# Kernel optimization log

Measured on AMD Instinct MI355X. Metric: run time of the kernel, lower is better.

The kernel has to match this reference:

```python
import jax, jax.numpy as jnp
import numpy as np

N = 100000   # nodes
E = 2000000  # edges per etype
D = 256      # in_dim
C = 16       # num_classes (per-etype Linear out dim)
R = 4        # number of canonical etypes


def setup_inputs() -> dict:
    key = jax.random.key(0)
    k0, k1, k2, k3, k4, k5 = jax.random.split(key, 6)
    feat = jax.random.normal(k0, (N, D), dtype=jnp.float32)
    src_idx = jax.random.randint(k1, (R, E), 0, N, dtype=jnp.int32)
    dst_idx = jax.random.randint(k2, (R, E), 0, N, dtype=jnp.int32)
    eweight = jax.random.uniform(k3, (R, E, 1), dtype=jnp.float32)
    W = jax.random.normal(k4, (R, D, C), dtype=jnp.float32) / np.sqrt(D).astype(np.float32)
    b = jax.random.normal(k5, (R, C), dtype=jnp.float32) * 0.01
    return {"feat": feat, "src_idx": src_idx, "dst_idx": dst_idx,
            "eweight": eweight, "W": W, "b": b}


def reference(feat, src_idx, dst_idx, eweight, W, b):
    """Hetero GNN layer: per-etype Linear -> u_mul_e message -> mean reduce per
    dst node -> sum across etypes (DGL multi_update_all(..., 'sum'))."""
    n = feat.shape[0]

    def per_etype(Wr, br, src, dst, ew):
        wh = feat @ Wr + br                      # [N, C] per-etype linear
        m = jnp.take(wh, src, axis=0) * ew       # [E, C] u_mul_e message
        s = jax.ops.segment_sum(m, dst, num_segments=n)            # [N, C]
        cnt = jax.ops.segment_sum(jnp.ones((src.shape[0],), feat.dtype),
                                  dst, num_segments=n)             # [N]
        # DGL mean: nodes with no incoming messages contribute 0
        cnt = cnt[:, None]
        return jnp.where(cnt > 0, s / jnp.maximum(cnt, 1.0), jnp.zeros_like(s))

    h = jax.vmap(per_etype)(W, b, src_idx, dst_idx, eweight)  # [R, N, C]
    return h.sum(axis=0)                                       # cross-etype sum
```

## Files before the change

### kernel.cpp

```cpp
#include <hip/hip_runtime.h>

constexpr int N = 100000;
constexpr int E = 2000000;
constexpr int D = 256;
constexpr int C = 16;
constexpr int R = 4;
constexpr int NCOL = R * C;
constexpr int TOT = R * E;

constexpr int BKN = 256;
constexpr int NBUK = (N + BKN - 1) / BKN;
constexpr int EPB = 16384;
constexpr int NBLK = (E + EPB - 1) / EPB;
constexpr int NROWS = R * NBUK;
constexpr int HLEN = NROWS * NBLK;
constexpr int SCAN_ELEMS = 2048;
constexpr int SCAN_NBLK = (HLEN + SCAN_ELEMS - 1) / SCAN_ELEMS;
constexpr int CAP = 3328;
constexpr int CHK = 4096;
constexpr int AGRID = ((NBUK + 1) / 2) * 8;
constexpr int SGRID = ((NBLK + 1) / 2) * 8;

typedef __attribute__((ext_vector_type(8))) short short8;
typedef __attribute__((ext_vector_type(8))) unsigned short u16x8;
typedef __attribute__((ext_vector_type(4))) float f32x4;
typedef __attribute__((ext_vector_type(4))) int i32x4;

__device__ __forceinline__ float bf2f(unsigned short h) {
    return __uint_as_float(((unsigned int)h) << 16);
}
__device__ __forceinline__ unsigned short f2bf(float f) {
    unsigned int x = __float_as_uint(f);
    x += 0x7FFFu + ((x >> 16) & 1u);
    return (unsigned short)(x >> 16);
}

__global__ void wt_kernel(const float* __restrict__ W, short8* __restrict__ wtb) {
    const int idx = blockIdx.x * blockDim.x + threadIdx.x;
    if (idx >= 8 * 4 * 64) return;
    const int lane = idx & 63;
    const int ct   = (idx >> 6) & 3;
    const int ks   = idx >> 8;
    const int r = ct, c = lane & 15;
    const int kbase = ks * 32 + (lane >> 4) * 8;
    short8 v;
#pragma unroll
    for (int j = 0; j < 8; ++j)
        v[j] = (short)f2bf(W[(size_t)r * D * C + (size_t)(kbase + j) * C + c]);
    wtb[idx] = v;
}

__global__ __launch_bounds__(256) void gemm_kernel(
    const f32x4* __restrict__ feat4, const short8* __restrict__ wtb,
    const float* __restrict__ b, unsigned short* __restrict__ whb) {
    __shared__ unsigned short alds[64 * 272];
    const int t   = threadIdx.x;
    const int n0  = blockIdx.x * 64;

#pragma unroll
    for (int j = 0; j < 16; ++j) {
        const int idx = t + j * 256;
        const int row = idx >> 6, k4 = idx & 63;
        const int grow = n0 + row;
        const int lrow = (grow < N) ? grow : (N - 1);
        const f32x4 v = __builtin_nontemporal_load(&feat4[(size_t)lrow * 64 + k4]);
        ushort4 u;
        u.x = f2bf(v.x); u.y = f2bf(v.y); u.z = f2bf(v.z); u.w = f2bf(v.w);
        *(ushort4*)&alds[row * 272 + k4 * 4] = u;
    }
    __syncthreads();

    const int lane = t & 63;
    const int wv   = t >> 6;
    const int wrow = wv * 16 + (lane & 15);
    const int kblk = lane >> 4;

    f32x4 acc0 = {0.f, 0.f, 0.f, 0.f};
    f32x4 acc1 = acc0, acc2 = acc0, acc3 = acc0;

#pragma unroll
    for (int ks = 0; ks < 8; ++ks) {
        const short8 af = *(const short8*)&alds[wrow * 272 + ks * 32 + kblk * 8];
        const short8 b0 = wtb[(ks * 4 + 0) * 64 + lane];
        const short8 b1 = wtb[(ks * 4 + 1) * 64 + lane];
        const short8 b2 = wtb[(ks * 4 + 2) * 64 + lane];
        const short8 b3 = wtb[(ks * 4 + 3) * 64 + lane];
        acc0 = __builtin_amdgcn_mfma_f32_16x16x32_bf16(af, b0, acc0, 0, 0, 0);
        acc1 = __builtin_amdgcn_mfma_f32_16x16x32_bf16(af, b1, acc1, 0, 0, 0);
        acc2 = __builtin_amdgcn_mfma_f32_16x16x32_bf16(af, b2, acc2, 0, 0, 0);
        acc3 = __builtin_amdgcn_mfma_f32_16x16x32_bf16(af, b3, acc3, 0, 0, 0);
    }

    const int c    = lane & 15;
    const int rowb = n0 + wv * 16 + (lane >> 4) * 4;
    const float bias0 = b[ 0 + c];
    const float bias1 = b[16 + c];
    const float bias2 = b[32 + c];
    const float bias3 = b[48 + c];
#pragma unroll
    for (int reg = 0; reg < 4; ++reg) {
        const int gr = rowb + reg;
        if (gr < N) {
            whb[((size_t)0 * N + gr) * 16 + c] = f2bf(acc0[reg] + bias0);
            whb[((size_t)1 * N + gr) * 16 + c] = f2bf(acc1[reg] + bias1);
            whb[((size_t)2 * N + gr) * 16 + c] = f2bf(acc2[reg] + bias2);
            whb[((size_t)3 * N + gr) * 16 + c] = f2bf(acc3[reg] + bias3);
        }
    }
}

__global__ __launch_bounds__(256) void hist_kernel(const int* __restrict__ dst,
                                                   int* __restrict__ hist) {
    __shared__ int hcnt[NBUK];
    const int t = threadIdx.x;
    const int r = blockIdx.y;
    for (int i = t; i < NBUK; i += 256) hcnt[i] = 0;
    __syncthreads();
    const int e0 = blockIdx.x * EPB;
    if (E - e0 >= EPB) {
        const i32x4* d4 = (const i32x4*)(dst + (size_t)r * E + e0);
#pragma unroll
        for (int j = 0; j < EPB / 1024; ++j) {
            const i32x4 d = __builtin_nontemporal_load(&d4[t + j * 256]);
            atomicAdd(&hcnt[d.x >> 8], 1);
            atomicAdd(&hcnt[d.y >> 8], 1);
            atomicAdd(&hcnt[d.z >> 8], 1);
            atomicAdd(&hcnt[d.w >> 8], 1);
        }
    } else {
        const int* d = dst + (size_t)r * E;
        for (int e = e0 + t; e < E; e += 256)
            atomicAdd(&hcnt[d[e] >> 8], 1);
    }
    __syncthreads();
    for (int i = t; i < NBUK; i += 256)
        hist[(size_t)(r * NBUK + i) * NBLK + blockIdx.x] = hcnt[i];
}

__global__ __launch_bounds__(256) void scan1_kernel(int* __restrict__ data,
                                                    int* __restrict__ partials) {
    __shared__ int sh[256];
    const int t = threadIdx.x;
    const int idx = blockIdx.x * SCAN_ELEMS + t * 8;
    int v[8];
#pragma unroll
    for (int j = 0; j < 8; ++j)
        v[j] = (idx + j < HLEN) ? data[idx + j] : 0;
    int s = 0;
#pragma unroll
    for (int j = 0; j < 8; ++j) s += v[j];
    sh[t] = s;
    __syncthreads();
    for (int off = 1; off < 256; off <<= 1) {
        int x = (t >= off) ? sh[t - off] : 0;
        __syncthreads();
        sh[t] += x;
        __syncthreads();
    }
    int run = sh[t] - s;
    if (t == 255) partials[blockIdx.x] = sh[255];
#pragma unroll
    for (int j = 0; j < 8; ++j) {
        if (idx + j < HLEN) data[idx + j] = run;
        run += v[j];
    }
}

__global__ __launch_bounds__(1024) void scan2_kernel(int* __restrict__ partials, int n) {
    __shared__ int sh[1024];
    const int t = threadIdx.x;
    int a = (2 * t     < n) ? partials[2 * t]     : 0;
    int b = (2 * t + 1 < n) ? partials[2 * t + 1] : 0;
    const int s = a + b;
    sh[t] = s;
    __syncthreads();
    for (int off = 1; off < 1024; off <<= 1) {
        int x = (t >= off) ? sh[t - off] : 0;
        __syncthreads();
        sh[t] += x;
        __syncthreads();
    }
    const int excl = sh[t] - s;
    if (2 * t     < n) partials[2 * t]     = excl;
    if (2 * t + 1 < n) partials[2 * t + 1] = excl + a;
}

__global__ void scan3_kernel(int* __restrict__ data, const int* __restrict__ partials) {
    const int i = blockIdx.x * blockDim.x + threadIdx.x;
    if (i < HLEN) data[i] += partials[i / SCAN_ELEMS];
}

__global__ __launch_bounds__(512) void scatter_kernel(const int* __restrict__ src,
                                                      const int* __restrict__ dst,
                                                      const float* __restrict__ ew,
                                                      const int* __restrict__ hist,
                                                      int2* __restrict__ sorted) {
    __shared__ int2 lrec[CHK];
    __shared__ int  lidx[CHK];
    __shared__ short lbkt[CHK];
    __shared__ int gcur[NBUK];
    __shared__ int loff[NBUK + 1];
    __shared__ int lcnt[NBUK];
    const int t = threadIdx.x;
    const int s = blockIdx.x & 7;
    const int r = s >> 1;
    const int cb0 = (blockIdx.x >> 3) * 2 + (s & 1);
    if (cb0 >= NBLK) return;

    for (int i = t; i < NBUK; i += 512)
        gcur[i] = hist[(size_t)(r * NBUK + i) * NBLK + cb0];

    const int e0 = cb0 * EPB;
    const int e1 = min(e0 + EPB, E);
    const int* sp = src + (size_t)r * E;
    const int* dp = dst + (size_t)r * E;
    const float* wp = ew + (size_t)r * E;

    for (int cb = e0; cb < e1; cb += CHK) {
        const int L = min(CHK, e1 - cb);
        for (int i = t; i < NBUK; i += 512) lcnt[i] = 0;
        __syncthreads();

        if (L == CHK) {
            const i32x4* s4 = (const i32x4*)(sp + cb);
            const i32x4* d4 = (const i32x4*)(dp + cb);
            const f32x4* w4 = (const f32x4*)(wp + cb);
#pragma unroll
            for (int j = 0; j < CHK / 2048; ++j) {
                const int v = t + j * 512;
                const i32x4 d = __builtin_nontemporal_load(&d4[v]);
                const i32x4 s2 = __builtin_nontemporal_load(&s4[v]);
                const f32x4 w = __builtin_nontemporal_load(&w4[v]);
#pragma unroll
                for (int q = 0; q < 4; ++q) {
                    const int dd = (q == 0) ? d.x : (q == 1) ? d.y : (q == 2) ? d.z : d.w;
                    const int ss = (q == 0) ? s2.x : (q == 1) ? s2.y : (q == 2) ? s2.z : s2.w;
                    const float ww = (q == 0) ? w.x : (q == 1) ? w.y : (q == 2) ? w.z : w.w;
                    const int b = dd >> 8;
                    int2 p;
                    p.x = ss | ((dd & 255) << 20);
                    p.y = __float_as_int(ww);
                    lrec[v * 4 + q] = p;
                    lbkt[v * 4 + q] = (short)b;
                    atomicAdd(&lcnt[b], 1);
                }
            }
        } else {
            for (int i = t; i < L; i += 512) {
                const int dd = dp[cb + i];
                const int ss = sp[cb + i];
                const float ww = wp[cb + i];
                const int b = dd >> 8;
                int2 p;
                p.x = ss | ((dd & 255) << 20);
                p.y = __float_as_int(ww);
                lrec[i] = p;
                lbkt[i] = (short)b;
                atomicAdd(&lcnt[b], 1);
            }
        }
        __syncthreads();

        for (int off = 1; off < NBUK; off <<= 1) {
            int x = 0;
            if (t < NBUK && t >= off) x = lcnt[t - off];
            __syncthreads();
            if (t < NBUK) lcnt[t] += x;
            __syncthreads();
        }
        if (t < NBUK) loff[t + 1] = lcnt[t];
        if (t == 0) loff[0] = 0;
        __syncthreads();
        if (t < NBUK) lcnt[t] = loff[t];
        __syncthreads();

        for (int i = t; i < L; i += 512) {
            const int b = lbkt[i];
            const int pos = atomicAdd(&lcnt[b], 1);
            lidx[pos] = i | (b << 16);
        }
        __syncthreads();

        for (int p = t; p < L; p += 512) {
            const int v = lidx[p];
            const int i = v & 0xFFFF;
            const int b = v >> 16;
            sorted[gcur[b] + (p - loff[b])] = lrec[i];
        }
        __syncthreads();

        for (int b = t; b < NBUK; b += 512)
            gcur[b] += loff[b + 1] - loff[b];
        __syncthreads();
    }
}

__global__ __launch_bounds__(512) void accum_kernel(const int2* __restrict__ sorted,
                                                    const u16x8* __restrict__ whb8,
                                                    const int* __restrict__ hist,
                                                    float* __restrict__ part) {
    __shared__ int2 lrec[CAP];
    __shared__ unsigned short lidx[CAP];
    __shared__ int loff[BKN + 1];
    __shared__ int lcur[BKN];
    const int t = threadIdx.x;
    const int s  = blockIdx.x & 7;
    const int r  = s >> 1;
    const int ck = (blockIdx.x >> 3) * 2 + (s & 1);
    if (ck >= NBUK) return;
    const int g = t >> 1, h = t & 1;

    const int row = r * NBUK + ck;
    const int start = hist[(size_t)row * NBLK];
    const int end   = (row + 1 < NROWS) ? hist[(size_t)(row + 1) * NBLK] : TOT;
    const int L = end - start;
    int L0 = (L + 1) >> 1; if (L0 > CAP) L0 = CAP;
    int L1 = L - L0;       if (L1 > CAP) L1 = CAP;

    const int wbase = r * N;
    float a0 = 0.f, a1 = 0.f, a2 = 0.f, a3 = 0.f;
    float a4 = 0.f, a5 = 0.f, a6 = 0.f, a7 = 0.f;
    int deg = 0;

    int pbase = start;
    int plen  = L0;
#pragma unroll
    for (int pass = 0; pass < 2; ++pass) {
        if (t < BKN) lcur[t] = 0;
        __syncthreads();

        for (int i = t; i < plen; i += 512) {
            long long raw = __builtin_nontemporal_load((const long long*)&sorted[pbase + i]);
            int2 p = *(int2*)&raw;
            lrec[i] = p;
            atomicAdd(&lcur[(p.x >> 20) & 255], 1);
        }
        __syncthreads();

        for (int off = 1; off < BKN; off <<= 1) {
            int x = 0;
            if (t < BKN && t >= off) x = lcur[t - off];
            __syncthreads();
            if (t < BKN) lcur[t] += x;
            __syncthreads();
        }
        if (t < BKN) loff[t + 1] = lcur[t];
        if (t == 0) loff[0] = 0;
        __syncthreads();
        if (t < BKN) lcur[t] = loff[t];
        __syncthreads();

        for (int i = t; i < plen; i += 512) {
            const int dl = (lrec[i].x >> 20) & 255;
            const int pos = atomicAdd(&lcur[dl], 1);
            lidx[pos] = (unsigned short)i;
        }
        __syncthreads();

        const int s0 = loff[g], e0 = loff[g + 1];
        deg += e0 - s0;

        int j = s0;
        for (; j + 4 <= e0; j += 4) {
            const int i0 = lidx[j], i1 = lidx[j + 1];
            const int i2 = lidx[j + 2], i3 = lidx[j + 3];
            const int2 r0 = lrec[i0], r1 = lrec[i1], r2 = lrec[i2], r3 = lrec[i3];
            const u16x8 u0 = whb8[(size_t)(wbase + (r0.x & 0xFFFFF)) * 2 + h];
            const u16x8 u1 = whb8[(size_t)(wbase + (r1.x & 0xFFFFF)) * 2 + h];
            const u16x8 u2 = whb8[(size_t)(wbase + (r2.x & 0xFFFFF)) * 2 + h];
            const u16x8 u3 = whb8[(size_t)(wbase + (r3.x & 0xFFFFF)) * 2 + h];
            const float w0 = __int_as_float(r0.y), w1 = __int_as_float(r1.y);
            const float w2 = __int_as_float(r2.y), w3 = __int_as_float(r3.y);
            a0 += bf2f(u0[0]) * w0 + bf2f(u1[0]) * w1 + bf2f(u2[0]) * w2 + bf2f(u3[0]) * w3;
            a1 += bf2f(u0[1]) * w0 + bf2f(u1[1]) * w1 + bf2f(u2[1]) * w2 + bf2f(u3[1]) * w3;
            a2 += bf2f(u0[2]) * w0 + bf2f(u1[2]) * w1 + bf2f(u2[2]) * w2 + bf2f(u3[2]) * w3;
            a3 += bf2f(u0[3]) * w0 + bf2f(u1[3]) * w1 + bf2f(u2[3]) * w2 + bf2f(u3[3]) * w3;
            a4 += bf2f(u0[4]) * w0 + bf2f(u1[4]) * w1 + bf2f(u2[4]) * w2 + bf2f(u3[4]) * w3;
            a5 += bf2f(u0[5]) * w0 + bf2f(u1[5]) * w1 + bf2f(u2[5]) * w2 + bf2f(u3[5]) * w3;
            a6 += bf2f(u0[6]) * w0 + bf2f(u1[6]) * w1 + bf2f(u2[6]) * w2 + bf2f(u3[6]) * w3;
            a7 += bf2f(u0[7]) * w0 + bf2f(u1[7]) * w1 + bf2f(u2[7]) * w2 + bf2f(u3[7]) * w3;
        }
        for (; j < e0; ++j) {
            const int2 r0 = lrec[lidx[j]];
            const u16x8 u0 = whb8[(size_t)(wbase + (r0.x & 0xFFFFF)) * 2 + h];
            const float w0 = __int_as_float(r0.y);
            a0 += bf2f(u0[0]) * w0; a1 += bf2f(u0[1]) * w0;
            a2 += bf2f(u0[2]) * w0; a3 += bf2f(u0[3]) * w0;
            a4 += bf2f(u0[4]) * w0; a5 += bf2f(u0[5]) * w0;
            a6 += bf2f(u0[6]) * w0; a7 += bf2f(u0[7]) * w0;
        }
        __syncthreads();

        pbase += plen;
        plen = L1;
    }

    const int node = ck * BKN + g;
    if (node < N) {
        const float inv = (deg > 0) ? 1.f / (float)deg : 0.f;
        float4 v0, v1;
        v0.x = a0 * inv; v0.y = a1 * inv; v0.z = a2 * inv; v0.w = a3 * inv;
        v1.x = a4 * inv; v1.y = a5 * inv; v1.z = a6 * inv; v1.w = a7 * inv;
        float* op = &part[(size_t)(wbase + node) * 16 + h * 8];
        *(float4*)op = v0;
        *(float4*)(op + 4) = v1;
    }
}

__global__ void finalize_kernel(const float4* __restrict__ part4,
                                float4* __restrict__ out4) {
    const int i = blockIdx.x * blockDim.x + threadIdx.x;
    if (i >= N * 4) return;
    float4 a = part4[i];
    const float4 b = part4[(size_t)N * 4 + i];
    const float4 c = part4[(size_t)2 * N * 4 + i];
    const float4 d = part4[(size_t)3 * N * 4 + i];
    a.x += b.x + c.x + d.x;
    a.y += b.y + c.y + d.y;
    a.z += b.z + c.z + d.z;
    a.w += b.w + c.w + d.w;
    out4[i] = a;
}

extern "C" void kernel_launch(void* const* d_in, const int* in_sizes, int n_in,
                              void* d_out, int out_size, void* d_ws, size_t ws_size,
                              hipStream_t stream) {
    const float* feat = (const float*)d_in[0];
    const int*   src  = (const int*)d_in[1];
    const int*   dst  = (const int*)d_in[2];
    const float* ew   = (const float*)d_in[3];
    const float* W    = (const float*)d_in[4];
    const float* b    = (const float*)d_in[5];
    float* out = (float*)d_out;

    char* base = (char*)d_ws;
    int2*           sorted   = (int2*)base;           base += (size_t)TOT * 8;
    short8*         wtb      = (short8*)base;         base += (size_t)64 * NCOL * 16;
    unsigned short* whb      = (unsigned short*)base; base += (size_t)R * N * C * 2;
    int*            hist     = (int*)base;            base += (size_t)HLEN * 4;
    int*            partials = (int*)base;            base += (size_t)4096;
    float*          part     = (float*)base;

    wt_kernel<<<8, 256, 0, stream>>>(W, wtb);
    gemm_kernel<<<(N + 63) / 64, 256, 0, stream>>>((const f32x4*)feat, wtb, b, whb);

    hist_kernel<<<dim3(NBLK, R), 256, 0, stream>>>(dst, hist);
    scan1_kernel<<<SCAN_NBLK, 256, 0, stream>>>(hist, partials);
    scan2_kernel<<<1, 1024, 0, stream>>>(partials, SCAN_NBLK);
    scan3_kernel<<<(HLEN + 255) / 256, 256, 0, stream>>>(hist, partials);

    scatter_kernel<<<SGRID, 512, 0, stream>>>(src, dst, ew, hist, sorted);
    accum_kernel<<<AGRID, 512, 0, stream>>>(sorted, (const u16x8*)whb, hist, part);
    finalize_kernel<<<(N * 4 + 255) / 256, 256, 0, stream>>>((const float4*)part, (float4*)out);
}
```

Before: 177.8 us.

## Dynamically assign dst nodes to thread pairs and use wave-shuffle scan

Inside accum_kernel, the fixed mapping of each thread pair to one destination node is replaced by dynamic scheduling: pairs take node indices from a shared atomic counter and add their partial sums into a shared-memory tile plus a degree array. This is meant to cut load imbalance from skewed per-node in-degrees within a bucket. The 256-entry block scan, which used many __syncthreads rounds, becomes a single-wave shuffle scan with 4 elements per lane. In exchange it adds shared-memory traffic, 16 KB more LDS per block (which may lower occupancy), and per-node atomics.

```diff
diff --git a/kernel.cpp b/kernel.cpp
--- a/kernel.cpp
+++ b/kernel.cpp
@@ -301,14 +301,18 @@
                                                     float* __restrict__ part) {
     __shared__ int2 lrec[CAP];
     __shared__ unsigned short lidx[CAP];
+    __shared__ float tile[BKN * 16];
+    __shared__ int degs[BKN];
     __shared__ int loff[BKN + 1];
     __shared__ int lcur[BKN];
+    __shared__ int nextg;
     const int t = threadIdx.x;
     const int s  = blockIdx.x & 7;
     const int r  = s >> 1;
     const int ck = (blockIdx.x >> 3) * 2 + (s & 1);
     if (ck >= NBUK) return;
-    const int g = t >> 1, h = t & 1;
+    const int lane = t & 63;
+    const int h = t & 1;
 
     const int row = r * NBUK + ck;
     const int start = hist[(size_t)row * NBLK];
@@ -318,15 +322,16 @@
     int L1 = L - L0;       if (L1 > CAP) L1 = CAP;
 
     const int wbase = r * N;
-    float a0 = 0.f, a1 = 0.f, a2 = 0.f, a3 = 0.f;
-    float a4 = 0.f, a5 = 0.f, a6 = 0.f, a7 = 0.f;
-    int deg = 0;
+
+    for (int i = t; i < BKN * 16; i += 512) tile[i] = 0.f;
+    if (t < BKN) degs[t] = 0;
 
     int pbase = start;
     int plen  = L0;
 #pragma unroll
     for (int pass = 0; pass < 2; ++pass) {
         if (t < BKN) lcur[t] = 0;
+        if (t == 0) nextg = 0;
         __syncthreads();
 
         for (int i = t; i < plen; i += 512) {
@@ -337,17 +342,23 @@
         }
         __syncthreads();
 
-        for (int off = 1; off < BKN; off <<= 1) {
-            int x = 0;
-            if (t < BKN && t >= off) x = lcur[t - off];
-            __syncthreads();
-            if (t < BKN) lcur[t] += x;
-            __syncthreads();
-        }
-        if (t < BKN) loff[t + 1] = lcur[t];
-        if (t == 0) loff[0] = 0;
-        __syncthreads();
-        if (t < BKN) lcur[t] = loff[t];
+        if (t < 64) {
+            const int b0 = lcur[4 * t], b1 = lcur[4 * t + 1];
+            const int b2 = lcur[4 * t + 2], b3 = lcur[4 * t + 3];
+            const int ssum = b0 + b1 + b2 + b3;
+            int incl = ssum;
+#pragma unroll
+            for (int off = 1; off < 64; off <<= 1) {
+                const int x = __shfl_up(incl, off, 64);
+                if (t >= off) incl += x;
+            }
+            const int excl = incl - ssum;
+            loff[4 * t]     = excl;                lcur[4 * t]     = excl;
+            loff[4 * t + 1] = excl + b0;           lcur[4 * t + 1] = excl + b0;
+            loff[4 * t + 2] = excl + b0 + b1;      lcur[4 * t + 2] = excl + b0 + b1;
+            loff[4 * t + 3] = excl + b0 + b1 + b2; lcur[4 * t + 3] = excl + b0 + b1 + b2;
+            if (t == 63) loff[BKN] = incl;
+        }
         __syncthreads();
 
         for (int i = t; i < plen; i += 512) {
@@ -357,37 +368,57 @@
         }
         __syncthreads();
 
-        const int s0 = loff[g], e0 = loff[g + 1];
-        deg += e0 - s0;
-
-        int j = s0;
-        for (; j + 4 <= e0; j += 4) {
-            const int i0 = lidx[j], i1 = lidx[j + 1];
-            const int i2 = lidx[j + 2], i3 = lidx[j + 3];
-            const int2 r0 = lrec[i0], r1 = lrec[i1], r2 = lrec[i2], r3 = lrec[i3];
-            const u16x8 u0 = whb8[(size_t)(wbase + (r0.x & 0xFFFFF)) * 2 + h];
-            const u16x8 u1 = whb8[(size_t)(wbase + (r1.x & 0xFFFFF)) * 2 + h];
-            const u16x8 u2 = whb8[(size_t)(wbase + (r2.x & 0xFFFFF)) * 2 + h];
-            const u16x8 u3 = whb8[(size_t)(wbase + (r3.x & 0xFFFFF)) * 2 + h];
-            const float w0 = __int_as_float(r0.y), w1 = __int_as_float(r1.y);
-            const float w2 = __int_as_float(r2.y), w3 = __int_as_float(r3.y);
-            a0 += bf2f(u0[0]) * w0 + bf2f(u1[0]) * w1 + bf2f(u2[0]) * w2 + bf2f(u3[0]) * w3;
-            a1 += bf2f(u0[1]) * w0 + bf2f(u1[1]) * w1 + bf2f(u2[1]) * w2 + bf2f(u3[1]) * w3;
-            a2 += bf2f(u0[2]) * w0 + bf2f(u1[2]) * w1 + bf2f(u2[2]) * w2 + bf2f(u3[2]) * w3;
-            a3 += bf2f(u0[3]) * w0 + bf2f(u1[3]) * w1 + bf2f(u2[3]) * w2 + bf2f(u3[3]) * w3;
-            a4 += bf2f(u0[4]) * w0 + bf2f(u1[4]) * w1 + bf2f(u2[4]) * w2 + bf2f(u3[4]) * w3;
-            a5 += bf2f(u0[5]) * w0 + bf2f(u1[5]) * w1 + bf2f(u2[5]) * w2 + bf2f(u3[5]) * w3;
-            a6 += bf2f(u0[6]) * w0 + bf2f(u1[6]) * w1 + bf2f(u2[6]) * w2 + bf2f(u3[6]) * w3;
-            a7 += bf2f(u0[7]) * w0 + bf2f(u1[7]) * w1 + bf2f(u2[7]) * w2 + bf2f(u3[7]) * w3;
-        }
-        for (; j < e0; ++j) {
-            const int2 r0 = lrec[lidx[j]];
-            const u16x8 u0 = whb8[(size_t)(wbase + (r0.x & 0xFFFFF)) * 2 + h];
-            const float w0 = __int_as_float(r0.y);
-            a0 += bf2f(u0[0]) * w0; a1 += bf2f(u0[1]) * w0;
-            a2 += bf2f(u0[2]) * w0; a3 += bf2f(u0[3]) * w0;
-            a4 += bf2f(u0[4]) * w0; a5 += bf2f(u0[5]) * w0;
-            a6 += bf2f(u0[6]) * w0; a7 += bf2f(u0[7]) * w0;
+        const int evenlane = lane & ~1;
+        while (true) {
+            int n = 0;
+            if (h == 0) n = atomicAdd(&nextg, 1);
+            n = __shfl(n, evenlane, 64);
+            const bool active = (n < BKN);
+            if (__all(!active)) break;
+            if (active) {
+                const int s0 = loff[n], e0 = loff[n + 1];
+
+                float a0 = 0.f, a1 = 0.f, a2 = 0.f, a3 = 0.f;
+                float a4 = 0.f, a5 = 0.f, a6 = 0.f, a7 = 0.f;
+                int j = s0;
+                for (; j + 4 <= e0; j += 4) {
+                    const int i0 = lidx[j], i1 = lidx[j + 1];
+                    const int i2 = lidx[j + 2], i3 = lidx[j + 3];
+                    const int2 r0 = lrec[i0], r1 = lrec[i1], r2 = lrec[i2], r3 = lrec[i3];
+                    const u16x8 u0 = whb8[(size_t)(wbase + (r0.x & 0xFFFFF)) * 2 + h];
+                    const u16x8 u1 = whb8[(size_t)(wbase + (r1.x & 0xFFFFF)) * 2 + h];
+                    const u16x8 u2 = whb8[(size_t)(wbase + (r2.x & 0xFFFFF)) * 2 + h];
+                    const u16x8 u3 = whb8[(size_t)(wbase + (r3.x & 0xFFFFF)) * 2 + h];
+                    const float w0 = __int_as_float(r0.y), w1 = __int_as_float(r1.y);
+                    const float w2 = __int_as_float(r2.y), w3 = __int_as_float(r3.y);
+                    a0 += bf2f(u0[0]) * w0 + bf2f(u1[0]) * w1 + bf2f(u2[0]) * w2 + bf2f(u3[0]) * w3;
+                    a1 += bf2f(u0[1]) * w0 + bf2f(u1[1]) * w1 + bf2f(u2[1]) * w2 + bf2f(u3[1]) * w3;
+                    a2 += bf2f(u0[2]) * w0 + bf2f(u1[2]) * w1 + bf2f(u2[2]) * w2 + bf2f(u3[2]) * w3;
+                    a3 += bf2f(u0[3]) * w0 + bf2f(u1[3]) * w1 + bf2f(u2[3]) * w2 + bf2f(u3[3]) * w3;
+                    a4 += bf2f(u0[4]) * w0 + bf2f(u1[4]) * w1 + bf2f(u2[4]) * w2 + bf2f(u3[4]) * w3;
+                    a5 += bf2f(u0[5]) * w0 + bf2f(u1[5]) * w1 + bf2f(u2[5]) * w2 + bf2f(u3[5]) * w3;
+                    a6 += bf2f(u0[6]) * w0 + bf2f(u1[6]) * w1 + bf2f(u2[6]) * w2 + bf2f(u3[6]) * w3;
+                    a7 += bf2f(u0[7]) * w0 + bf2f(u1[7]) * w1 + bf2f(u2[7]) * w2 + bf2f(u3[7]) * w3;
+                }
+                for (; j < e0; ++j) {
+                    const int2 r0 = lrec[lidx[j]];
+                    const u16x8 u0 = whb8[(size_t)(wbase + (r0.x & 0xFFFFF)) * 2 + h];
+                    const float w0 = __int_as_float(r0.y);
+                    a0 += bf2f(u0[0]) * w0; a1 += bf2f(u0[1]) * w0;
+                    a2 += bf2f(u0[2]) * w0; a3 += bf2f(u0[3]) * w0;
+                    a4 += bf2f(u0[4]) * w0; a5 += bf2f(u0[5]) * w0;
+                    a6 += bf2f(u0[6]) * w0; a7 += bf2f(u0[7]) * w0;
+                }
+
+                float* tp = &tile[n * 16 + h * 8];
+                float4 v0 = *(float4*)tp;
+                float4 v1 = *(float4*)(tp + 4);
+                v0.x += a0; v0.y += a1; v0.z += a2; v0.w += a3;
+                v1.x += a4; v1.y += a5; v1.z += a6; v1.w += a7;
+                *(float4*)tp = v0;
+                *(float4*)(tp + 4) = v1;
+                if (h == 0) degs[n] += e0 - s0;
+            }
         }
         __syncthreads();
 
@@ -395,12 +426,15 @@
         plen = L1;
     }
 
-    const int node = ck * BKN + g;
+    const int g2 = t >> 1;
+    const int node = ck * BKN + g2;
     if (node < N) {
+        const int deg = degs[g2];
         const float inv = (deg > 0) ? 1.f / (float)deg : 0.f;
+        const float* tp = &tile[g2 * 16 + h * 8];
         float4 v0, v1;
-        v0.x = a0 * inv; v0.y = a1 * inv; v0.z = a2 * inv; v0.w = a3 * inv;
-        v1.x = a4 * inv; v1.y = a5 * inv; v1.z = a6 * inv; v1.w = a7 * inv;
+        v0.x = tp[0] * inv; v0.y = tp[1] * inv; v0.z = tp[2] * inv; v0.w = tp[3] * inv;
+        v1.x = tp[4] * inv; v1.y = tp[5] * inv; v1.z = tp[6] * inv; v1.w = tp[7] * inv;
         float* op = &part[(size_t)(wbase + node) * 16 + h * 8];
         *(float4*)op = v0;
         *(float4*)(op + 4) = v1;
```

Result: no change. 176.4 us (-0.8%).
